# Kernel tuning notes

Hardware: AMD Instinct MI355X
Metric: run time of the kernel (lower is better)

Reference implementation:

```python
import jax, jax.numpy as jnp
import numpy as np

DIM = 512
HID = 1024        # dim * expansion_factor
QK = 128          # query_key_dim
G = 256           # group_size
EPS = 1e-5


def setup_inputs() -> dict:
    key = jax.random.key(0)
    ks = jax.random.split(key, 6)
    x = jax.random.normal(ks[0], (4, 4096, DIM), jnp.float32)
    ln_w = jnp.ones((DIM,), jnp.float32)
    ln_b = jnp.zeros((DIM,), jnp.float32)
    Wh = 0.02 * jax.random.normal(ks[1], (DIM, 2 * HID), jnp.float32)
    bh = jnp.zeros((2 * HID,), jnp.float32)
    Wqk = 0.02 * jax.random.normal(ks[2], (DIM, QK), jnp.float32)
    bqk = jnp.zeros((QK,), jnp.float32)
    gamma = 0.02 * jax.random.normal(ks[3], (4, QK), jnp.float32)  # nn.init.normal_(gamma, std=0.02)
    beta = jnp.zeros((4, QK), jnp.float32)
    Wo = 0.02 * jax.random.normal(ks[4], (HID, DIM), jnp.float32)
    bo = jnp.zeros((DIM,), jnp.float32)
    return {"x": x, "ln_w": ln_w, "ln_b": ln_b, "Wh": Wh, "bh": bh,
            "Wqk": Wqk, "bqk": bqk, "gamma": gamma, "beta": beta,
            "Wo": Wo, "bo": bo}


def reference(x, ln_w, ln_b, Wh, bh, Wqk, bqk, gamma, beta, Wo, bo):
    b, n, _ = x.shape
    g = n // G  # number of groups (n chosen as multiple of G -> no padding)

    # LayerNorm (torch uses biased variance)
    mu = jnp.mean(x, axis=-1, keepdims=True)
    var = jnp.mean((x - mu) ** 2, axis=-1, keepdims=True)
    normed = (x - mu) * jax.lax.rsqrt(var + EPS) * ln_w + ln_b

    # to_hidden: Linear -> SiLU, split into v / gate
    h = jax.nn.silu(normed @ Wh + bh)            # [b, n, 2*HID]
    v, gate = jnp.split(h, 2, axis=-1)           # each [b, n, HID]

    # to_qk: Linear -> SiLU, then 4-head offset/scale
    qk = jax.nn.silu(normed @ Wqk + bqk)         # [b, n, QK]
    qkh = qk[..., None, :] * gamma + beta        # [b, n, 4, QK]
    quad_q, lin_q, quad_k, lin_k = (qkh[..., i, :] for i in range(4))

    # group: b (g n) d -> b g n d
    grp = lambda t: t.reshape(b, g, G, t.shape[-1])
    qq, qk_, lq, lk, vv = map(grp, (quad_q, quad_k, lin_q, lin_k, v))

    # quadratic (group-local) attention with ReLU^2 scores, causal within group
    sim = jnp.einsum('bgid,bgjd->bgij', qq, qk_) / G
    attn = jnp.square(jnp.maximum(sim, 0.0))
    causal_mask = jnp.triu(jnp.ones((G, G), dtype=bool), 1)
    attn = jnp.where(causal_mask, 0.0, attn)
    quad_out = jnp.einsum('bgij,bgje->bgie', attn, vv)   # [b, g, G, HID]

    # linear attention across groups: per-group kv, exclusive cumsum over group dim
    lin_kv = jnp.einsum('bgnd,bgne->bgde', lk, vv) / G   # [b, g, QK, HID]
    lin_kv = jnp.cumsum(lin_kv, axis=1)
    lin_kv = jnp.pad(lin_kv, ((0, 0), (1, 0), (0, 0), (0, 0)))[:, :-1]
    lin_out = jnp.einsum('bgde,bgnd->bgne', lin_kv, lq)  # [b, g, G, HID]

    out = gate * (quad_out.reshape(b, n, HID) + lin_out.reshape(b, n, HID))
    return out @ Wo + bo + x
```

## Files before the change

### kernel.cpp

```cpp
#include <hip/hip_runtime.h>
#include <hip/hip_bf16.h>
#include <math.h>


#define BATCH 4
#define SEQ   4096
#define TROWS 16384
#define DIMD  512
#define HIDD  1024
#define QKD   128
#define GRP   256
#define NGRP  16
#define BGRP  64
#define EPIW  132
#define EPB   130

typedef unsigned short bfraw;
typedef __attribute__((ext_vector_type(8))) short bf16x8;
typedef __attribute__((ext_vector_type(8))) unsigned short u16x8;
typedef __attribute__((ext_vector_type(4))) unsigned int u32x4;
typedef __attribute__((ext_vector_type(4))) float f32x4;

__device__ __forceinline__ float bf2f(bfraw u) {
    union { float f; unsigned int i; } c;
    c.i = ((unsigned int)u) << 16;
    return c.f;
}
__device__ __forceinline__ bfraw f2bf(float f) {
    unsigned int x = __float_as_uint(f);
    unsigned int r = (x + 0x7fffu + ((x >> 16) & 1u)) >> 16;
    return (bfraw)r;
}
__device__ __forceinline__ unsigned int pkbf(float lo, float hi) {
    __hip_bfloat162 h2 = __float22bfloat162_rn(make_float2(lo, hi));
    union { __hip_bfloat162 h; unsigned int u; } c; c.h = h2;
    return c.u;
}
__device__ __forceinline__ void store16bf(bfraw* dst, const float* src) {
    u32x4 a, b;
    #pragma unroll
    for (int k = 0; k < 4; ++k) a[k] = pkbf(src[2 * k], src[2 * k + 1]);
    #pragma unroll
    for (int k = 0; k < 4; ++k) b[k] = pkbf(src[8 + 2 * k], src[8 + 2 * k + 1]);
    *(u32x4*)dst = a;
    *(u32x4*)(dst + 8) = b;
}
__device__ __forceinline__ void store8bf(bfraw* dst, const float* src) {
    u32x4 a;
    #pragma unroll
    for (int k = 0; k < 4; ++k) a[k] = pkbf(src[2 * k], src[2 * k + 1]);
    *(u32x4*)dst = a;
}
__device__ __forceinline__ float silu_f(float z) {
    return z / (1.f + __expf(-z));
}
__device__ __forceinline__ void gload_lds16(const void* g, void* l) {
    __builtin_amdgcn_global_load_lds(
        (const __attribute__((address_space(1))) unsigned int*)g,
        (__attribute__((address_space(3))) unsigned int*)l, 16, 0, 0);
}

__device__ __forceinline__ void mfma_step(const bfraw* As, const bfraw* Bs,
                                          f32x4 acc[4][4], int wm, int wn,
                                          int q, int mi) {
    bf16x8 af[4], bfg[4];
    #pragma unroll
    for (int i = 0; i < 4; ++i)
        af[i] = *(const bf16x8*)&As[(size_t)(wm * 64 + i * 16 + mi) * 32 + q * 8];
    #pragma unroll
    for (int j = 0; j < 4; ++j)
        bfg[j] = *(const bf16x8*)&Bs[(size_t)(wn * 64 + j * 16 + mi) * 32 + q * 8];
    #pragma unroll
    for (int i = 0; i < 4; ++i)
        #pragma unroll
        for (int j = 0; j < 4; ++j)
            acc[i][j] = __builtin_amdgcn_mfma_f32_16x16x32_bf16(af[i], bfg[j], acc[i][j], 0, 0, 0);
}

#define SMEMP_DECL                                              \
    __shared__ __align__(16) char smem_[33280];                 \
    bfraw* A0buf = (bfraw*)smem_;                               \
    bfraw* B0buf = (bfraw*)(smem_ + 8192);                      \
    bfraw* A1buf = (bfraw*)(smem_ + 16384);                     \
    bfraw* B1buf = (bfraw*)(smem_ + 24576);

#define PIPE_DSTS                                               \
    bfraw* a0d  = A0buf + wid * 512;                            \
    bfraw* a0d2 = A0buf + 2048 + wid * 512;                     \
    bfraw* b0d  = B0buf + wid * 512;                            \
    bfraw* b0d2 = B0buf + 2048 + wid * 512;                     \
    bfraw* a1d  = A1buf + wid * 512;                            \
    bfraw* a1d2 = A1buf + 2048 + wid * 512;                     \
    bfraw* b1d  = B1buf + wid * 512;                            \
    bfraw* b1d2 = B1buf + 2048 + wid * 512;

#define KLOOP_PRE(Abase, Astr, Bbase, Bstr)                                    \
    const bfraw* pa0 = (Abase) + (size_t)(t >> 2) * (Astr) + (t & 3) * 8;      \
    const bfraw* pa1 = pa0 + (size_t)64 * (Astr);                              \
    const bfraw* pb0 = (Bbase) + (size_t)(t >> 2) * (Bstr) + (t & 3) * 8;      \
    const bfraw* pb1 = pb0 + (size_t)64 * (Bstr);

#define STAGE0                                                                 \
    do { gload_lds16(pa0, a0d); gload_lds16(pa1, a0d2);                        \
         gload_lds16(pb0, b0d); gload_lds16(pb1, b0d2);                        \
         pa0 += 32; pa1 += 32; pb0 += 32; pb1 += 32; } while (0)
#define STAGE1                                                                 \
    do { gload_lds16(pa0, a1d); gload_lds16(pa1, a1d2);                        \
         gload_lds16(pb0, b1d); gload_lds16(pb1, b1d2);                        \
         pa0 += 32; pa1 += 32; pb0 += 32; pb1 += 32; } while (0)

#define PIPE_LOOP(NIT, Abase, Astr, Bbase, Bstr)                               \
    {                                                                          \
        KLOOP_PRE(Abase, Astr, Bbase, Bstr)                                    \
        STAGE0;                                                                \
        for (int it = 0; it < (NIT); it += 2) {                                \
            __syncthreads();                                                   \
            if (it + 1 < (NIT)) STAGE1;                                        \
            mfma_step(A0buf, B0buf, acc, wm, wn, q, mi);                       \
            __syncthreads();                                                   \
            if (it + 2 < (NIT)) STAGE0;                                        \
            if (it + 1 < (NIT))                                                \
                mfma_step(A1buf, B1buf, acc, wm, wn, q, mi);                   \
        }                                                                      \
        __syncthreads();                                                       \
    }

__device__ __forceinline__ int epi_row(int p, int lr) {
    return (lr < 16) ? (p * 16 + lr) : (64 + p * 16 + (lr - 16));
}

__global__ __launch_bounds__(256) void prep_kernel(const float* __restrict__ x,
                                                   const float* __restrict__ lnw,
                                                   const float* __restrict__ lnb,
                                                   const float* __restrict__ Wh,
                                                   const float* __restrict__ Wo,
                                                   const float* __restrict__ Wqk,
                                                   bfraw* __restrict__ normb,
                                                   bfraw* __restrict__ WhT,
                                                   bfraw* __restrict__ WoT,
                                                   bfraw* __restrict__ WqkT) {
    __shared__ float tile[32][33];
    int bid = blockIdx.x;
    int t = threadIdx.x;
    if (bid < 4096) {
        int row  = bid * 4 + (t >> 6);
        int lane = t & 63;
        const float* xr = x + (size_t)row * DIMD;
        float4 v0 = ((const float4*)xr)[lane];
        float4 v1 = ((const float4*)xr)[lane + 64];
        float s  = v0.x + v0.y + v0.z + v0.w + v1.x + v1.y + v1.z + v1.w;
        float ss = v0.x*v0.x + v0.y*v0.y + v0.z*v0.z + v0.w*v0.w
                 + v1.x*v1.x + v1.y*v1.y + v1.z*v1.z + v1.w*v1.w;
        #pragma unroll
        for (int off = 32; off; off >>= 1) {
            s  += __shfl_xor(s, off);
            ss += __shfl_xor(ss, off);
        }
        float mu  = s * (1.f / DIMD);
        float var = ss * (1.f / DIMD) - mu * mu;
        float inv = rsqrtf(var + 1e-5f);
        float4 w0 = ((const float4*)lnw)[lane],  w1 = ((const float4*)lnw)[lane + 64];
        float4 b0 = ((const float4*)lnb)[lane],  b1 = ((const float4*)lnb)[lane + 64];
        unsigned int o0 = pkbf((v0.x - mu) * inv * w0.x + b0.x,
                               (v0.y - mu) * inv * w0.y + b0.y);
        unsigned int o1 = pkbf((v0.z - mu) * inv * w0.z + b0.z,
                               (v0.w - mu) * inv * w0.w + b0.w);
        unsigned int o2 = pkbf((v1.x - mu) * inv * w1.x + b1.x,
                               (v1.y - mu) * inv * w1.y + b1.y);
        unsigned int o3 = pkbf((v1.z - mu) * inv * w1.z + b1.z,
                               (v1.w - mu) * inv * w1.w + b1.w);
        unsigned int* brow = (unsigned int*)(normb + (size_t)row * DIMD);
        ((uint2*)brow)[lane]      = make_uint2(o0, o1);
        ((uint2*)brow)[lane + 64] = make_uint2(o2, o3);
        return;
    }
    bid -= 4096;
    const float* in; bfraw* outp; int R, C, nx;
    if (bid < 1024)      { in = Wh;  outp = WhT;  R = DIMD; C = 2 * HIDD; nx = 64; }
    else if (bid < 1536) { bid -= 1024; in = Wo;  outp = WoT;  R = HIDD; C = DIMD; nx = 16; }
    else                 { bid -= 1536; in = Wqk; outp = WqkT; R = DIMD; C = QKD;  nx = 4; }
    int c0 = (bid % nx) * 32, r0 = (bid / nx) * 32;
    int tr = t >> 3, tc4 = (t & 7) * 4;
    float4 v = *(const float4*)&in[(size_t)(r0 + tr) * C + c0 + tc4];
    tile[tr][tc4 + 0] = v.x; tile[tr][tc4 + 1] = v.y;
    tile[tr][tc4 + 2] = v.z; tile[tr][tc4 + 3] = v.w;
    __syncthreads();
    ushort4 s;
    s.x = f2bf(tile[tc4 + 0][tr]);
    s.y = f2bf(tile[tc4 + 1][tr]);
    s.z = f2bf(tile[tc4 + 2][tr]);
    s.w = f2bf(tile[tc4 + 3][tr]);
    *(ushort4*)&outp[(size_t)(c0 + tr) * R + r0 + tc4] = s;
}

__global__ __launch_bounds__(512, 4) void gemm_h256(
    const bfraw* __restrict__ A,
    const bfraw* __restrict__ WhT,
    const bfraw* __restrict__ WqkT,
    const float* __restrict__ bh,
    const float* __restrict__ bqk,
    const float* __restrict__ gamma,
    const float* __restrict__ beta,
    bfraw* __restrict__ vT,
    bfraw* __restrict__ gate,
    bfraw* __restrict__ qq,
    bfraw* __restrict__ lq,
    bfraw* __restrict__ kk,
    bfraw* __restrict__ lkT) {
    __shared__ __align__(16) char smem_[73728];
    const int t = threadIdx.x;
    const int lane = t & 63, wid = t >> 6;
    const int wm = wid >> 2, wn = wid & 3;
    const int q = lane >> 4, mi = lane & 15;
    int nid = (blockIdx.x & 7) * 144 + (blockIdx.x >> 3);
    const int ct = nid % 9, by = nid / 9;
    const int r0 = by * 128, c0 = ct * 256;
    const int bg = r0 >> 8;
    const int jb0 = r0 & 255;

    const int lslot = (t & 7) ^ ((t >> 3) & 7);
    const int srow  = 2 * (t >> 3) + (lslot >> 2);
    const int skel  = (lslot & 3) * 8;
    const bfraw* Asrc = A + (size_t)(r0 + srow) * DIMD + skel;
    const bfraw* Bsrc0;
    const bfraw* Bsrc1;
    if (ct < 8) {
        Bsrc0 = WhT + (size_t)(c0 + srow) * DIMD + skel;
        Bsrc1 = Bsrc0 + (size_t)128 * DIMD;
    } else {
        Bsrc0 = WqkT + (size_t)srow * DIMD + skel;
        Bsrc1 = Bsrc0;
    }
    const int swz = ((((mi & 1) << 2) | q) ^ ((mi >> 1) & 7)) << 4;
    const int a_off = (wm * 32 + (mi >> 1)) * 128 + swz;
    const int b_off = (wn * 32 + (mi >> 1)) * 128 + swz;

#define GH_STAGE(KT, SLOT)                                                    \
    do {                                                                      \
        char* sb_ = smem_ + (SLOT) * 24576;                                   \
        gload_lds16(Asrc  + (KT) * 32, sb_ + t * 16);                         \
        gload_lds16(Bsrc0 + (KT) * 32, sb_ + 8192 + t * 16);                  \
        gload_lds16(Bsrc1 + (KT) * 32, sb_ + 16384 + t * 16);                 \
    } while (0)

    f32x4 acc[4][4] = {};
    GH_STAGE(0, 0);
    GH_STAGE(1, 1);
    asm volatile("s_waitcnt vmcnt(3)" ::: "memory");
    __builtin_amdgcn_s_barrier();

    #pragma unroll
    for (int j = 0; j < 16; ++j) {
        if (j + 2 < 16) GH_STAGE(j + 2, (j + 2) % 3);
        const char* cb = smem_ + (j % 3) * 24576;
        bf16x8 af[4], bfr[4];
        #pragma unroll
        for (int mf = 0; mf < 4; ++mf)
            af[mf] = *(const bf16x8*)(cb + a_off + mf * 1024);
        #pragma unroll
        for (int nf = 0; nf < 4; ++nf)
            bfr[nf] = *(const bf16x8*)(cb + 8192 + b_off + nf * 1024);
        __builtin_amdgcn_s_setprio(1);
        #pragma unroll
        for (int mf = 0; mf < 4; ++mf)
            #pragma unroll
            for (int nf = 0; nf < 4; ++nf)
                acc[mf][nf] = __builtin_amdgcn_mfma_f32_16x16x32_bf16(
                    af[mf], bfr[nf], acc[mf][nf], 0, 0, 0);
        __builtin_amdgcn_s_setprio(0);
        if (j + 2 < 16)      asm volatile("s_waitcnt vmcnt(3)" ::: "memory");
        else if (j + 1 < 16) asm volatile("s_waitcnt vmcnt(0)" ::: "memory");
        __builtin_amdgcn_s_barrier();
    }
#undef GH_STAGE

    float* epi = (float*)smem_;
    if (ct == 8) {
        float* gbl = (float*)(smem_ + 36864);
        gbl[t] = gamma[t];
        gbl[t + 512] = beta[t];
        float bq4[4];
        #pragma unroll
        for (int nf = 0; nf < 4; ++nf)
            bq4[nf] = (wn < 2) ? bqk[wn * 64 + nf * 16 + mi] : 0.f;
        #pragma unroll
        for (int p2 = 0; p2 < 4; ++p2) {
            if (wm == (p2 >> 1) && wn < 2) {
                #pragma unroll
                for (int mf2 = 0; mf2 < 2; ++mf2) {
                    int mf = ((p2 & 1) << 1) + mf2;
                    #pragma unroll
                    for (int nf = 0; nf < 4; ++nf)
                        #pragma unroll
                        for (int rg = 0; rg < 4; ++rg)
                            epi[(mf2 * 16 + q * 4 + rg) * 132 + wn * 64 + nf * 16 + mi] =
                                silu_f(acc[mf][nf][rg] + bq4[nf]);
                }
            }
            __syncthreads();
            {
                int lr = t >> 4, cs = (t & 15) * 8;
                float z[8];
                #pragma unroll
                for (int k = 0; k < 8; ++k) z[k] = epi[lr * 132 + cs + k];
                size_t growr = (size_t)(r0 + p2 * 32 + lr) * QKD + cs;
                #pragma unroll
                for (int hd = 0; hd < 3; ++hd) {
                    bfraw* arr = (hd == 0) ? qq : (hd == 1) ? lq : kk;
                    float tmp[8];
                    #pragma unroll
                    for (int k = 0; k < 8; ++k)
                        tmp[k] = z[k] * gbl[hd * 128 + cs + k] + gbl[512 + hd * 128 + cs + k];
                    store8bf(arr + growr, tmp);
                }
            }
            {
                int c = t >> 2, jh = (t & 3) * 8;
                float g3 = gbl[384 + c], e3 = gbl[896 + c];
                float tmp[8];
                #pragma unroll
                for (int k = 0; k < 8; ++k)
                    tmp[k] = epi[(jh + k) * 132 + c] * g3 + e3;
                store8bf(lkT + ((size_t)bg * QKD + c) * GRP + jb0 + p2 * 32 + jh, tmp);
            }
            __syncthreads();
        }
        return;
    }
    float bias4[4];
    #pragma unroll
    for (int nf = 0; nf < 4; ++nf)
        bias4[nf] = bh[c0 + wn * 64 + nf * 16 + mi];
    if (ct < 4) {
        #pragma unroll
        for (int p2 = 0; p2 < 4; ++p2) {
            if (wm == (p2 >> 1)) {
                #pragma unroll
                for (int mf2 = 0; mf2 < 2; ++mf2) {
                    int mf = ((p2 & 1) << 1) + mf2;
                    #pragma unroll
                    for (int nf = 0; nf < 4; ++nf)
                        #pragma unroll
                        for (int rg = 0; rg < 4; ++rg)
                            epi[(mf2 * 16 + q * 4 + rg) * 257 + wn * 64 + nf * 16 + mi] =
                                silu_f(acc[mf][nf][rg] + bias4[nf]);
                }
            }
            __syncthreads();
            int e2 = t >> 1, js = (t & 1) * 16;
            float tmp[16];
            #pragma unroll
            for (int k = 0; k < 16; ++k)
                tmp[k] = epi[(js + k) * 257 + e2];
            store16bf(vT + ((size_t)bg * HIDD + c0 + e2) * GRP + jb0 + p2 * 32 + js, tmp);
            __syncthreads();
        }
    } else {
        #pragma unroll
        for (int p2 = 0; p2 < 4; ++p2) {
            if (wm == (p2 >> 1)) {
                #pragma unroll
                for (int mf2 = 0; mf2 < 2; ++mf2) {
                    int mf = ((p2 & 1) << 1) + mf2;
                    #pragma unroll
                    for (int nf = 0; nf < 4; ++nf)
                        #pragma unroll
                        for (int rg = 0; rg < 4; ++rg)
                            epi[(mf2 * 16 + q * 4 + rg) * 260 + wn * 64 + nf * 16 + mi] =
                                silu_f(acc[mf][nf][rg] + bias4[nf]);
                }
            }
            __syncthreads();
            int lr = t >> 4, cs = (t & 15) * 16;
            float tmp[16];
            #pragma unroll
            for (int k = 0; k < 16; ++k)
                tmp[k] = epi[lr * 260 + cs + k];
            store16bf(gate + (size_t)(r0 + p2 * 32 + lr) * HIDD + (c0 - HIDD) + cs, tmp);
            __syncthreads();
        }
    }
}

__global__ __launch_bounds__(256) void simkv_kernel(const bfraw* __restrict__ qq,
                                                    const bfraw* __restrict__ kk,
                                                    bfraw* __restrict__ attn,
                                                    const bfraw* __restrict__ vT,
                                                    const bfraw* __restrict__ lkT,
                                                    bfraw* __restrict__ kvT_raw) {
    SMEMP_DECL
    float* epi = (float*)smem_;
    int t = threadIdx.x;
    int lane = t & 63, wid = t >> 6;
    int wm = wid >> 1, wn = wid & 1;
    int q = lane >> 4, mi = lane & 15;
    int bid = blockIdx.x;
    f32x4 acc[4][4] = {};
    PIPE_DSTS
    if (bid < 512) {
        int bg = bid >> 3;
        int row0 = (bid & 7) * 128;
        PIPE_LOOP(8, vT + (size_t)bg * HIDD * GRP + (size_t)row0 * GRP, GRP,
                  lkT + (size_t)bg * QKD * GRP, GRP)
        bfraw* outg = kvT_raw + (size_t)bg * HIDD * QKD;
        #pragma unroll
        for (int p = 0; p < 4; ++p) {
            #pragma unroll
            for (int j = 0; j < 4; ++j)
                #pragma unroll
                for (int rg = 0; rg < 4; ++rg)
                    epi[(wm * 16 + q * 4 + rg) * EPIW + wn * 64 + j * 16 + mi] = acc[p][j][rg];
            __syncthreads();
            int lr = t >> 3, c0t = (t & 7) * 16;
            int gr = row0 + epi_row(p, lr);
            store16bf(outg + (size_t)gr * QKD + c0t, &epi[lr * EPIW + c0t]);
            __syncthreads();
        }
        return;
    }
    int i = bid - 512;
    int bg = i & 63;
    int tid = i >> 6;
    int ry = (tid == 0) ? 0 : 1;
    int rx = (tid == 2) ? 1 : 0;
    int row0 = ry * 128, col0 = rx * 128;
    PIPE_LOOP(4, qq + (size_t)(bg * GRP + row0) * QKD, QKD,
              kk + (size_t)(bg * GRP + col0) * QKD, QKD)
    bfraw* ag = attn + (size_t)bg * GRP * GRP;
    #pragma unroll
    for (int p = 0; p < 4; ++p) {
        #pragma unroll
        for (int j = 0; j < 4; ++j) {
            int colg = col0 + wn * 64 + j * 16 + mi;
            #pragma unroll
            for (int rg = 0; rg < 4; ++rg) {
                int rowg = row0 + wm * 64 + p * 16 + q * 4 + rg;
                float s = acc[p][j][rg] * (1.f / GRP);
                s = fmaxf(s, 0.f);
                s = s * s;
                epi[(wm * 16 + q * 4 + rg) * EPIW + wn * 64 + j * 16 + mi] =
                    (colg > rowg) ? 0.f : s;
            }
        }
        __syncthreads();
        int lr = t >> 3, c0t = (t & 7) * 16;
        int gr = row0 + epi_row(p, lr);
        store16bf(ag + (size_t)gr * GRP + col0 + c0t, &epi[lr * EPIW + c0t]);
        __syncthreads();
    }
}

__global__ __launch_bounds__(256) void cumsum2_kernel(const bfraw* __restrict__ raw,
                                                      bfraw* __restrict__ ex) {
    int idx = blockIdx.x * 256 + threadIdx.x;
    int b = idx >> 17;
    int r = idx & 131071;
    const bfraw* rp = raw + (size_t)b * NGRP * 131072 + r;
    bfraw* ep = ex + (size_t)b * NGRP * 131072 + r;
    float run = 0.f;
    #pragma unroll
    for (int g = 0; g < NGRP; ++g) {
        ep[(size_t)g * 131072] = f2bf(run);
        run += bf2f(rp[(size_t)g * 131072]) * (1.f / GRP);
    }
}

__global__ __launch_bounds__(256) void quadlin_mfma(const bfraw* __restrict__ attn,
                                                    const bfraw* __restrict__ vT,
                                                    const bfraw* __restrict__ lq,
                                                    const bfraw* __restrict__ kvT_ex,
                                                    const bfraw* __restrict__ gate,
                                                    bfraw* __restrict__ gated) {
    int bg = blockIdx.z;
    int row0 = blockIdx.y * 128;
    int col0 = blockIdx.x * 128;
    SMEMP_DECL
    float* epi = (float*)smem_;
    int t = threadIdx.x;
    int lane = t & 63, wid = t >> 6;
    int wm = wid >> 1, wn = wid & 1;
    int q = lane >> 4, mi = lane & 15;
    f32x4 acc[4][4] = {};
    PIPE_DSTS
    {
        int nit = (row0 + 128) >> 5;
        PIPE_LOOP(nit, attn + (size_t)bg * GRP * GRP + (size_t)row0 * GRP, GRP,
                  vT + (size_t)bg * HIDD * GRP + (size_t)col0 * GRP, GRP)
    }
    PIPE_LOOP(4, lq + (size_t)(bg * GRP + row0) * QKD, QKD,
              kvT_ex + (size_t)bg * HIDD * QKD + (size_t)col0 * QKD, QKD)
    #pragma unroll
    for (int p = 0; p < 4; ++p) {
        #pragma unroll
        for (int j = 0; j < 4; ++j)
            #pragma unroll
            for (int rg = 0; rg < 4; ++rg)
                epi[(wm * 16 + q * 4 + rg) * EPIW + wn * 64 + j * 16 + mi] = acc[p][j][rg];
        __syncthreads();
        int lr = t >> 3, c0t = (t & 7) * 16;
        int gr = row0 + epi_row(p, lr);
        size_t grow = (size_t)bg * GRP + gr;
        const float* src = &epi[lr * EPIW + c0t];
        const bfraw* gsrc = gate + grow * HIDD + col0 + c0t;
        u16x8 g0 = *(const u16x8*)gsrc;
        u16x8 g1 = *(const u16x8*)(gsrc + 8);
        float tmp[16];
        #pragma unroll
        for (int k = 0; k < 8; ++k) tmp[k] = src[k] * bf2f(g0[k]);
        #pragma unroll
        for (int k = 0; k < 8; ++k) tmp[8 + k] = src[8 + k] * bf2f(g1[k]);
        store16bf(gated + grow * HIDD + col0 + c0t, tmp);
        __syncthreads();
    }
}

__global__ __launch_bounds__(1024, 4) void gemm_final(
    const bfraw* __restrict__ A,
    const bfraw* __restrict__ BT,
    const float* __restrict__ bo,
    const float* __restrict__ x,
    float* __restrict__ out) {
    __shared__ __align__(16) char smem_[147456];
    const int t = threadIdx.x;
    const int lane = t & 63, wid = t >> 6;
    const int wm = wid >> 2, wn = wid & 3;
    const int q = lane >> 4, mi = lane & 15;
    int nid = (blockIdx.x & 7) * 32 + (blockIdx.x >> 3);
    const int by = nid >> 2, cx = nid & 3;
    const int r0 = by * 256, c0 = cx * 128;

    const int lslot = (t & 7) ^ ((t >> 3) & 7);
    const int a_row = 2 * (t >> 3) + (lslot >> 2);
    const int a_kel = (lslot & 3) * 8;
    const bfraw* Asrc = A + (size_t)(r0 + a_row) * HIDD + a_kel;
    const int u = t & 511;
    const int lsb = (u & 7) ^ ((u >> 3) & 7);
    const int b_row = 2 * (u >> 3) + (lsb >> 2);
    const int b_kel = (lsb & 3) * 8 + (t >> 9) * 32;
    const bfraw* Bsrc = BT + (size_t)(c0 + b_row) * HIDD + b_kel;

    const int swz = ((((mi & 1) << 2) | q) ^ ((mi >> 1) & 7)) << 4;
    const int a_off = (wm * 32 + (mi >> 1)) * 128 + swz;
    const int b_off = (wn * 16 + (mi >> 1)) * 128 + swz;

#define GF_STAGE(SS, SLOT)                                                    \
    do {                                                                      \
        char* sb_ = smem_ + (SLOT) * 49152;                                   \
        gload_lds16(Asrc + (SS) * 64,      sb_ + t * 16);                     \
        gload_lds16(Asrc + (SS) * 64 + 32, sb_ + 16384 + t * 16);             \
        gload_lds16(Bsrc + (SS) * 64,      sb_ + 32768 + t * 16);             \
    } while (0)

    f32x4 acc[4][2] = {};
    GF_STAGE(0, 0);
    GF_STAGE(1, 1);
    asm volatile("s_waitcnt vmcnt(3)" ::: "memory");
    __builtin_amdgcn_s_barrier();

    #pragma unroll
    for (int ss = 0; ss < 16; ++ss) {
        if (ss + 2 < 16) GF_STAGE(ss + 2, (ss + 2) % 3);
        const char* cb = smem_ + (ss % 3) * 49152;
        #pragma unroll
        for (int h = 0; h < 2; ++h) {
            bf16x8 af[4], bfr[2];
            #pragma unroll
            for (int mf = 0; mf < 4; ++mf)
                af[mf] = *(const bf16x8*)(cb + h * 16384 + a_off + mf * 1024);
            #pragma unroll
            for (int nf = 0; nf < 2; ++nf)
                bfr[nf] = *(const bf16x8*)(cb + 32768 + h * 8192 + b_off + nf * 1024);
            __builtin_amdgcn_s_setprio(1);
            #pragma unroll
            for (int mf = 0; mf < 4; ++mf)
                #pragma unroll
                for (int nf = 0; nf < 2; ++nf)
                    acc[mf][nf] = __builtin_amdgcn_mfma_f32_16x16x32_bf16(
                        af[mf], bfr[nf], acc[mf][nf], 0, 0, 0);
            __builtin_amdgcn_s_setprio(0);
        }
        if (ss + 2 < 16)      asm volatile("s_waitcnt vmcnt(3)" ::: "memory");
        else if (ss + 1 < 16) asm volatile("s_waitcnt vmcnt(0)" ::: "memory");
        __builtin_amdgcn_s_barrier();
    }
#undef GF_STAGE

    float* epi = (float*)smem_;
    float bo2[2];
    #pragma unroll
    for (int nf = 0; nf < 2; ++nf)
        bo2[nf] = bo[c0 + wn * 32 + nf * 16 + mi];
    #pragma unroll
    for (int p = 0; p < 4; ++p) {
        if (wm == p) {
            #pragma unroll
            for (int mf = 0; mf < 4; ++mf)
                #pragma unroll
                for (int nf = 0; nf < 2; ++nf)
                    #pragma unroll
                    for (int rg = 0; rg < 4; ++rg)
                        epi[(mf * 16 + q * 4 + rg) * 132 + wn * 32 + nf * 16 + mi] =
                            acc[mf][nf][rg] + bo2[nf];
        }
        __syncthreads();
        int lr = t >> 4, cs = (t & 15) * 8;
        const float* src = epi + lr * 132 + cs;
        const float* xs = x + (size_t)(r0 + p * 64 + lr) * DIMD + c0 + cs;
        float* dst = out + (size_t)(r0 + p * 64 + lr) * DIMD + c0 + cs;
        #pragma unroll
        for (int v = 0; v < 2; ++v) {
            float4 a = ((const float4*)src)[v];
            float4 xv = ((const float4*)xs)[v];
            a.x += xv.x; a.y += xv.y; a.z += xv.z; a.w += xv.w;
            ((float4*)dst)[v] = a;
        }
        __syncthreads();
    }
}

extern "C" void kernel_launch(void* const* d_in, const int* in_sizes, int n_in,
                              void* d_out, int out_size, void* d_ws, size_t ws_size,
                              hipStream_t stream) {
    const float* x     = (const float*)d_in[0];
    const float* ln_w  = (const float*)d_in[1];
    const float* ln_b  = (const float*)d_in[2];
    const float* Wh    = (const float*)d_in[3];
    const float* bh    = (const float*)d_in[4];
    const float* Wqk   = (const float*)d_in[5];
    const float* bqk   = (const float*)d_in[6];
    const float* gamma = (const float*)d_in[7];
    const float* beta  = (const float*)d_in[8];
    const float* Wo    = (const float*)d_in[9];
    const float* bo    = (const float*)d_in[10];
    float* out = (float*)d_out;

    char* outb_ = (char*)d_out;
    bfraw* attn = (bfraw*)(outb_);
    bfraw* qq   = (bfraw*)(outb_ + 8388608);
    bfraw* kk   = (bfraw*)(outb_ + 12582912);
    bfraw* lq   = (bfraw*)(outb_ + 16777216);
    bfraw* WhT  = (bfraw*)(outb_ + 20971520);
    bfraw* WqkT = (bfraw*)(outb_ + 23068672);

    char* wsb = (char*)d_ws;
    bfraw* vT      = (bfraw*)(wsb);
    bfraw* gate    = (bfraw*)(wsb + 33554432);
    bfraw* gated   = (bfraw*)(wsb + 67108864);
    bfraw* normb   = (bfraw*)(wsb + 100663296);
    bfraw* kvT_raw = (bfraw*)(wsb + 117440512);
    bfraw* kvT_ex  = (bfraw*)(wsb + 134217728);
    bfraw* lkT     = (bfraw*)(wsb + 150994944);
    bfraw* WoT     = (bfraw*)(wsb + 155189248);

    prep_kernel<<<4096 + 1024 + 512 + 64, 256, 0, stream>>>(
        x, ln_w, ln_b, Wh, Wo, Wqk, normb, WhT, WoT, WqkT);
    gemm_h256<<<1152, 512, 0, stream>>>(
        normb, WhT, WqkT, bh, bqk, gamma, beta, vT, gate, qq, lq, kk, lkT);
    simkv_kernel<<<512 + 192, 256, 0, stream>>>(qq, kk, attn, vT, lkT, kvT_raw);
    cumsum2_kernel<<<(BATCH * QKD * HIDD) / 256, 256, 0, stream>>>(kvT_raw, kvT_ex);
    quadlin_mfma<<<dim3(HIDD / 128, GRP / 128, BGRP), 256, 0, stream>>>(
        attn, vT, lq, kvT_ex, gate, gated);
    gemm_final<<<256, 1024, 0, stream>>>(gated, WoT, bo, x, out);
}
```

Measured before the change: 257.7 us.

## Widen quad+linear attention tiles to 128x256 with triple-buffered LDS pipeline

Replaces the 128x128-tile, 256-thread quadlin kernel with a 512-thread kernel computing 128x256 output tiles. Loads go straight to LDS with an XOR-swizzled layout and a three-stage ring of buffers, and MFMA issue runs at raised wave priority. Block IDs are remapped so neighbouring blocks share an attention group. The wider tile reuses each attn/lq A-tile across twice as many columns, cutting global traffic, at the cost of more LDS per block and fewer blocks in flight.

```diff
diff --git a/kernel.cpp b/kernel.cpp
--- a/kernel.cpp
+++ b/kernel.cpp
@@ -465,43 +465,112 @@
     }
 }
 
-__global__ __launch_bounds__(256) void quadlin_mfma(const bfraw* __restrict__ attn,
-                                                    const bfraw* __restrict__ vT,
-                                                    const bfraw* __restrict__ lq,
-                                                    const bfraw* __restrict__ kvT_ex,
-                                                    const bfraw* __restrict__ gate,
-                                                    bfraw* __restrict__ gated) {
-    int bg = blockIdx.z;
-    int row0 = blockIdx.y * 128;
-    int col0 = blockIdx.x * 128;
-    SMEMP_DECL
+__global__ __launch_bounds__(512, 4) void quadlin256(
+    const bfraw* __restrict__ attn,
+    const bfraw* __restrict__ vT,
+    const bfraw* __restrict__ lq,
+    const bfraw* __restrict__ kvT_ex,
+    const bfraw* __restrict__ gate,
+    bfraw* __restrict__ gated) {
+    __shared__ __align__(16) char smem_[73728];
+    const int t = threadIdx.x;
+    const int lane = t & 63, wid = t >> 6;
+    const int wm = wid >> 2, wn = wid & 3;
+    const int q = lane >> 4, mi = lane & 15;
+    int nid = (blockIdx.x & 7) * 64 + (blockIdx.x >> 3);
+    const int bg = nid >> 3;
+    const int row0 = ((nid >> 2) & 1) * 128;
+    const int c0 = (nid & 3) * 256;
+
+    const int lslot = (t & 7) ^ ((t >> 3) & 7);
+    const int srow  = 2 * (t >> 3) + (lslot >> 2);
+    const int skel  = (lslot & 3) * 8;
+    const bfraw* A1 = attn + ((size_t)bg * GRP + row0 + srow) * GRP + skel;
+    const bfraw* B1a = vT + ((size_t)bg * HIDD + c0 + srow) * GRP + skel;
+    const bfraw* B1b = B1a + (size_t)128 * GRP;
+    const bfraw* A2 = lq + ((size_t)bg * GRP + row0 + srow) * QKD + skel;
+    const bfraw* B2a = kvT_ex + ((size_t)bg * HIDD + c0 + srow) * QKD + skel;
+    const bfraw* B2b = B2a + (size_t)128 * QKD;
+
+    const int swz = ((((mi & 1) << 2) | q) ^ ((mi >> 1) & 7)) << 4;
+    const int a_off = (wm * 32 + (mi >> 1)) * 128 + swz;
+    const int b_off = (wn * 32 + (mi >> 1)) * 128 + swz;
+
+#define QL_STAGE(PA, PB0, PB1, KT, SLOT)                                      \
+    do {                                                                      \
+        char* sb_ = smem_ + (SLOT) * 24576;                                   \
+        gload_lds16((PA)  + (KT) * 32, sb_ + t * 16);                         \
+        gload_lds16((PB0) + (KT) * 32, sb_ + 8192 + t * 16);                  \
+        gload_lds16((PB1) + (KT) * 32, sb_ + 16384 + t * 16);                 \
+    } while (0)
+#define QL_MFMA(SLOT)                                                         \
+    do {                                                                      \
+        const char* cb = smem_ + (SLOT) * 24576;                              \
+        bf16x8 af[4], bfr[4];                                                 \
+        _Pragma("unroll")                                                     \
+        for (int mf = 0; mf < 4; ++mf)                                        \
+            af[mf] = *(const bf16x8*)(cb + a_off + mf * 1024);                \
+        _Pragma("unroll")                                                     \
+        for (int nf = 0; nf < 4; ++nf)                                        \
+            bfr[nf] = *(const bf16x8*)(cb + 8192 + b_off + nf * 1024);        \
+        __builtin_amdgcn_s_setprio(1);                                        \
+        _Pragma("unroll")                                                     \
+        for (int mf = 0; mf < 4; ++mf)                                        \
+            _Pragma("unroll")                                                 \
+            for (int nf = 0; nf < 4; ++nf)                                    \
+                acc[mf][nf] = __builtin_amdgcn_mfma_f32_16x16x32_bf16(        \
+                    af[mf], bfr[nf], acc[mf][nf], 0, 0, 0);                   \
+        __builtin_amdgcn_s_setprio(0);                                        \
+    } while (0)
+
+    f32x4 acc[4][4] = {};
+    const int nit1 = (row0 + 128) >> 5;
+    QL_STAGE(A1, B1a, B1b, 0, 0);
+    QL_STAGE(A1, B1a, B1b, 1, 1);
+    asm volatile("s_waitcnt vmcnt(3)" ::: "memory");
+    __builtin_amdgcn_s_barrier();
+    for (int j = 0; j < nit1; ++j) {
+        if (j + 2 < nit1) QL_STAGE(A1, B1a, B1b, j + 2, (j + 2) % 3);
+        QL_MFMA(j % 3);
+        if (j + 2 < nit1)      asm volatile("s_waitcnt vmcnt(3)" ::: "memory");
+        else if (j + 1 < nit1) asm volatile("s_waitcnt vmcnt(0)" ::: "memory");
+        __builtin_amdgcn_s_barrier();
+    }
+    QL_STAGE(A2, B2a, B2b, 0, 0);
+    QL_STAGE(A2, B2a, B2b, 1, 1);
+    asm volatile("s_waitcnt vmcnt(3)" ::: "memory");
+    __builtin_amdgcn_s_barrier();
+    #pragma unroll
+    for (int j = 0; j < 4; ++j) {
+        if (j + 2 < 4) QL_STAGE(A2, B2a, B2b, j + 2, (j + 2) % 3);
+        QL_MFMA(j % 3);
+        if (j + 2 < 4)      asm volatile("s_waitcnt vmcnt(3)" ::: "memory");
+        else if (j + 1 < 4) asm volatile("s_waitcnt vmcnt(0)" ::: "memory");
+        __builtin_amdgcn_s_barrier();
+    }
+#undef QL_STAGE
+#undef QL_MFMA
+
     float* epi = (float*)smem_;
-    int t = threadIdx.x;
-    int lane = t & 63, wid = t >> 6;
-    int wm = wid >> 1, wn = wid & 1;
-    int q = lane >> 4, mi = lane & 15;
-    f32x4 acc[4][4] = {};
-    PIPE_DSTS
-    {
-        int nit = (row0 + 128) >> 5;
-        PIPE_LOOP(nit, attn + (size_t)bg * GRP * GRP + (size_t)row0 * GRP, GRP,
-                  vT + (size_t)bg * HIDD * GRP + (size_t)col0 * GRP, GRP)
-    }
-    PIPE_LOOP(4, lq + (size_t)(bg * GRP + row0) * QKD, QKD,
-              kvT_ex + (size_t)bg * HIDD * QKD + (size_t)col0 * QKD, QKD)
-    #pragma unroll
-    for (int p = 0; p < 4; ++p) {
-        #pragma unroll
-        for (int j = 0; j < 4; ++j)
-            #pragma unroll
-            for (int rg = 0; rg < 4; ++rg)
-                epi[(wm * 16 + q * 4 + rg) * EPIW + wn * 64 + j * 16 + mi] = acc[p][j][rg];
+    #pragma unroll
+    for (int p2 = 0; p2 < 4; ++p2) {
+        if (wm == (p2 >> 1)) {
+            #pragma unroll
+            for (int mf2 = 0; mf2 < 2; ++mf2) {
+                int mf = ((p2 & 1) << 1) + mf2;
+                #pragma unroll
+                for (int nf = 0; nf < 4; ++nf)
+                    #pragma unroll
+                    for (int rg = 0; rg < 4; ++rg)
+                        epi[(mf2 * 16 + q * 4 + rg) * 260 + wn * 64 + nf * 16 + mi] =
+                            acc[mf][nf][rg];
+            }
+        }
         __syncthreads();
-        int lr = t >> 3, c0t = (t & 7) * 16;
-        int gr = row0 + epi_row(p, lr);
-        size_t grow = (size_t)bg * GRP + gr;
-        const float* src = &epi[lr * EPIW + c0t];
-        const bfraw* gsrc = gate + grow * HIDD + col0 + c0t;
+        int lr = t >> 4, cs = (t & 15) * 16;
+        size_t grow = (size_t)bg * GRP + row0 + p2 * 32 + lr;
+        const float* src = epi + lr * 260 + cs;
+        const bfraw* gsrc = gate + grow * HIDD + c0 + cs;
         u16x8 g0 = *(const u16x8*)gsrc;
         u16x8 g1 = *(const u16x8*)(gsrc + 8);
         float tmp[16];
@@ -509,7 +578,7 @@
         for (int k = 0; k < 8; ++k) tmp[k] = src[k] * bf2f(g0[k]);
         #pragma unroll
         for (int k = 0; k < 8; ++k) tmp[8 + k] = src[8 + k] * bf2f(g1[k]);
-        store16bf(gated + grow * HIDD + col0 + c0t, tmp);
+        store16bf(gated + grow * HIDD + c0 + cs, tmp);
         __syncthreads();
     }
 }
@@ -658,7 +727,6 @@
         normb, WhT, WqkT, bh, bqk, gamma, beta, vT, gate, qq, lq, kk, lkT);
     simkv_kernel<<<512 + 192, 256, 0, stream>>>(qq, kk, attn, vT, lkT, kvT_raw);
     cumsum2_kernel<<<(BATCH * QKD * HIDD) / 256, 256, 0, stream>>>(kvT_raw, kvT_ex);
-    quadlin_mfma<<<dim3(HIDD / 128, GRP / 128, BGRP), 256, 0, stream>>>(
-        attn, vT, lq, kvT_ex, gate, gated);
+    quadlin256<<<512, 512, 0, stream>>>(attn, vT, lq, kvT_ex, gate, gated);
     gemm_final<<<256, 1024, 0, stream>>>(gated, WoT, bo, x, out);
 }
```

Result: faster. 240.4 us (-6.7%).
